# Kernel tuning notes

Hardware: AMD Instinct MI355X
Metric: run time of the kernel (lower is better)

The kernel has to match this reference:

```python
import jax, jax.numpy as jnp
import numpy as np

N_LAYERS = 2  # args.n_layers


def expmap0(u):
    """Hyperboloid (K=1/c, c=1) exponential map at the origin.
    u: [N, d] Euclidean tangent vector (spatial part; time coord is 0).
    Returns [N, d+1] point on the hyperboloid: (cosh||u||, sinh||u||*u/||u||).
    This matches Hyperboloid.expmap0(proj_tan0(cat([zeros, u], -1))) with c=1.
    """
    theta = jnp.sqrt(jnp.sum(u * u, axis=-1, keepdims=True))
    theta = jnp.maximum(theta, 1e-7)
    x0 = jnp.cosh(theta)
    xs = jnp.sinh(theta) * (u / theta)
    return jnp.concatenate([x0, xs], axis=-1)


def setup_inputs() -> dict:
    key = jax.random.key(0)
    k1, k2, k3, k4 = jax.random.split(key, 4)
    n_users, n_items, d, E = 100000, 150000, 64, 4000000
    N = n_users + n_items
    return {
        "user_emb": jax.random.normal(k1, (n_users, d), jnp.float32) * 0.1,
        "item_emb": jax.random.normal(k2, (n_items, d), jnp.float32) * 0.1,
        "h_list": jax.random.randint(k3, (E,), 0, N, dtype=jnp.int32),
        "t_list": jax.random.randint(k4, (E,), 0, N, dtype=jnp.int32),
    }


def reference(user_emb, item_emb, h_list, t_list):
    N = user_emb.shape[0] + item_emb.shape[0]
    dtype = user_emb.dtype

    # _cal_sparse_adj: symmetric normalization G = D^-1/2 A D^-1/2 in COO form
    deg = jax.ops.segment_sum(jnp.ones_like(h_list, dtype), h_list, num_segments=N)
    deg = jnp.maximum(deg, 1.0)
    g_values = jax.lax.rsqrt(deg[h_list] * deg[t_list])  # [E]

    # LightGCN-style propagation: x_{l+1} = G @ x_l, layer sum / mean
    x = jnp.concatenate([user_emb, item_emb], axis=0)  # [N, d]
    out = x
    for _ in range(N_LAYERS):
        msg = g_values[:, None] * x[t_list]              # [E, d] gather
        x = jax.ops.segment_sum(msg, h_list, num_segments=N)  # scatter-add SpMM
        out = out + x
    out = out / (N_LAYERS + 1)

    # Hyperbolic lift of the aggregated embeddings (zerou/zeroi + expmap0, c=1)
    h = expmap0(out)  # [N, d+1]

    return jnp.concatenate([out, h], axis=-1)  # [N, 2d+1]
```

## Files before the change

kernel.cpp:

```cpp
#include <hip/hip_runtime.h>

#define DIM 64
#define CHUNK 16384
#define BSHIFT 9
#define BSIZE (1 << BSHIFT)
#define MAXB 512
#define TBITS 21
#define TMASK ((1u << TBITS) - 1u)

__device__ __forceinline__ unsigned f2bf(float f) {
    unsigned u = __float_as_uint(f);
    return (u + 0x7FFFu + ((u >> 16) & 1u)) >> 16;
}
__device__ __forceinline__ float bflo(unsigned u) {
    return __uint_as_float(u << 16);
}
__device__ __forceinline__ float bfhi(unsigned u) {
    return __uint_as_float(u & 0xFFFF0000u);
}

__global__ void zero_u32(unsigned* __restrict__ p, int n) {
    int i = blockIdx.x * blockDim.x + threadIdx.x;
    int stride = gridDim.x * blockDim.x;
    for (; i < n; i += stride) p[i] = 0u;
}

__global__ void bucket_hist(const int* __restrict__ h, unsigned* __restrict__ bcount,
                            int E, int nb) {
    __shared__ unsigned s[MAXB];
    for (int i = threadIdx.x; i < nb; i += blockDim.x) s[i] = 0u;
    __syncthreads();
    int i = blockIdx.x * blockDim.x + threadIdx.x;
    int stride = gridDim.x * blockDim.x;
    for (; i < E; i += stride) atomicAdd(&s[((unsigned)h[i]) >> BSHIFT], 1u);
    __syncthreads();
    for (int i = threadIdx.x; i < nb; i += blockDim.x)
        if (s[i]) atomicAdd(&bcount[i], s[i]);
}

__global__ void bucket_scan(const unsigned* __restrict__ bcount,
                            unsigned* __restrict__ bbase, unsigned* __restrict__ bcur,
                            unsigned* __restrict__ row_ptr, int nb, int N, int E) {
    __shared__ unsigned s[MAXB];
    int tid = threadIdx.x;
    unsigned v = (tid < nb) ? bcount[tid] : 0u;
    s[tid] = v; __syncthreads();
    for (int off = 1; off < MAXB; off <<= 1) {
        unsigned t = (tid >= off) ? s[tid - off] : 0u;
        __syncthreads();
        s[tid] += t; __syncthreads();
    }
    if (tid < nb) {
        unsigned ex = s[tid] - v;
        bbase[tid] = ex;
        bcur[tid] = ex;
    }
    if (tid == 0) {
        bbase[nb] = (unsigned)E;
        row_ptr[N] = (unsigned)E;
    }
}

__global__ void partition_edges(const int* __restrict__ h, const int* __restrict__ t,
                                unsigned* __restrict__ bcur, unsigned* __restrict__ tmp,
                                int E, int nb) {
    __shared__ unsigned cnt[MAXB];
    int tid = threadIdx.x;
    long start = (long)blockIdx.x * CHUNK;
    long end = start + CHUNK; if (end > E) end = E;
    for (int i = tid; i < nb; i += blockDim.x) cnt[i] = 0u;
    __syncthreads();
    for (long i = start + tid; i < end; i += blockDim.x)
        atomicAdd(&cnt[((unsigned)h[i]) >> BSHIFT], 1u);
    __syncthreads();
    for (int i = tid; i < nb; i += blockDim.x) {
        unsigned c = cnt[i];
        cnt[i] = c ? atomicAdd(&bcur[i], c) : 0u;
    }
    __syncthreads();
    for (long i = start + tid; i < end; i += blockDim.x) {
        unsigned hn = (unsigned)h[i], tn = (unsigned)t[i];
        unsigned pos = atomicAdd(&cnt[hn >> BSHIFT], 1u);
        tmp[pos] = ((hn & (BSIZE - 1)) << TBITS) | tn;
    }
}

__global__ void build_csr_bucket(const unsigned* __restrict__ tmp,
                                 const unsigned* __restrict__ bbase,
                                 unsigned* __restrict__ row_ptr,
                                 float* __restrict__ rdeg,
                                 float* __restrict__ rsq,
                                 int* __restrict__ col,
                                 const float* __restrict__ ue,
                                 const float* __restrict__ ie,
                                 int n_users,
                                 unsigned short* __restrict__ x0s, int N) {
    __shared__ unsigned cnt[BSIZE];
    __shared__ unsigned cur[BSIZE];
    __shared__ unsigned ts[BSIZE];
    int b = blockIdx.x;
    int tid = threadIdx.x;
    unsigned e0 = bbase[b], e1 = bbase[b + 1];
    int nlo = b << BSHIFT;
    int nloc = N - nlo; if (nloc > BSIZE) nloc = BSIZE;
    cnt[tid] = 0u;
    __syncthreads();
    for (unsigned i = e0 + tid; i < e1; i += BSIZE)
        atomicAdd(&cnt[tmp[i] >> TBITS], 1u);
    __syncthreads();
    unsigned myc = cnt[tid];
    ts[tid] = myc; __syncthreads();
    for (int off = 1; off < BSIZE; off <<= 1) {
        unsigned t = (tid >= off) ? ts[tid - off] : 0u;
        __syncthreads();
        ts[tid] += t; __syncthreads();
    }
    unsigned off0 = ts[tid] - myc;
    if (tid < nloc) {
        float d = fmaxf((float)myc, 1.0f);
        cur[tid] = off0;
        row_ptr[nlo + tid] = e0 + off0;
        rdeg[nlo + tid] = rsqrtf(d);
        rsq[nlo + tid]  = sqrtf(d);
    }
    __syncthreads();
    for (unsigned i = e0 + tid; i < e1; i += BSIZE) {
        unsigned pk = tmp[i];
        unsigned pos = e0 + atomicAdd(&cur[pk >> TBITS], 1u);
        col[pos] = (int)(pk & TMASK);
    }
    long nu_elems = (long)n_users * DIM;
    int total = nloc * 16;
    for (int idx = tid; idx < total; idx += BSIZE) {
        int i = idx >> 4, j = idx & 15;
        long n = (long)(nlo + i);
        long elem = n * DIM + j * 4;
        const float* src = (elem < nu_elems) ? ue + elem : ie + (elem - nu_elems);
        float rd = rsqrtf(fmaxf((float)cnt[i], 1.0f));
        float4 v = *(const float4*)src;
        ushort4 o;
        o.x = (unsigned short)f2bf(rd * v.x); o.y = (unsigned short)f2bf(rd * v.y);
        o.z = (unsigned short)f2bf(rd * v.z); o.w = (unsigned short)f2bf(rd * v.w);
        *(ushort4*)(x0s + elem) = o;
    }
}

__global__ void spmm_pull_l1(const unsigned* __restrict__ rp,
                             const int* __restrict__ col,
                             const float* __restrict__ rdeg,
                             const uint4* __restrict__ x0s,
                             uint4* __restrict__ x1s, int N) {
    int node = blockIdx.x * (blockDim.x >> 3) + (threadIdx.x >> 3);
    int l = threadIdx.x & 7;
    if (node >= N) return;
    int e0 = (int)rp[node], e1 = (int)rp[node + 1];
    float a0 = 0.f, a1 = 0.f, a2 = 0.f, a3 = 0.f;
    float a4 = 0.f, a5 = 0.f, a6 = 0.f, a7 = 0.f;
    int e = e0;
    for (; e + 4 <= e1; e += 4) {
        int c0 = col[e], c1 = col[e + 1], c2 = col[e + 2], c3 = col[e + 3];
        uint4 u0 = x0s[((size_t)c0 << 3) + l];
        uint4 u1 = x0s[((size_t)c1 << 3) + l];
        uint4 u2 = x0s[((size_t)c2 << 3) + l];
        uint4 u3 = x0s[((size_t)c3 << 3) + l];
        a0 += bflo(u0.x) + bflo(u1.x) + bflo(u2.x) + bflo(u3.x);
        a1 += bfhi(u0.x) + bfhi(u1.x) + bfhi(u2.x) + bfhi(u3.x);
        a2 += bflo(u0.y) + bflo(u1.y) + bflo(u2.y) + bflo(u3.y);
        a3 += bfhi(u0.y) + bfhi(u1.y) + bfhi(u2.y) + bfhi(u3.y);
        a4 += bflo(u0.z) + bflo(u1.z) + bflo(u2.z) + bflo(u3.z);
        a5 += bfhi(u0.z) + bfhi(u1.z) + bfhi(u2.z) + bfhi(u3.z);
        a6 += bflo(u0.w) + bflo(u1.w) + bflo(u2.w) + bflo(u3.w);
        a7 += bfhi(u0.w) + bfhi(u1.w) + bfhi(u2.w) + bfhi(u3.w);
    }
    for (; e < e1; ++e) {
        int c = col[e];
        uint4 u = x0s[((size_t)c << 3) + l];
        a0 += bflo(u.x); a1 += bfhi(u.x);
        a2 += bflo(u.y); a3 += bfhi(u.y);
        a4 += bflo(u.z); a5 += bfhi(u.z);
        a6 += bflo(u.w); a7 += bfhi(u.w);
    }
    float rd = rdeg[node];
    float rd2 = rd * rd;
    uint4 o;
    o.x = (f2bf(rd2 * a1) << 16) | f2bf(rd2 * a0);
    o.y = (f2bf(rd2 * a3) << 16) | f2bf(rd2 * a2);
    o.z = (f2bf(rd2 * a5) << 16) | f2bf(rd2 * a4);
    o.w = (f2bf(rd2 * a7) << 16) | f2bf(rd2 * a6);
    x1s[((size_t)node << 3) + l] = o;
}

__global__ void spmm_l2_finalize(const unsigned* __restrict__ rp,
                                 const int* __restrict__ col,
                                 const float* __restrict__ rdeg,
                                 const float* __restrict__ rsq,
                                 const uint4* __restrict__ x0s,
                                 const uint4* __restrict__ x1s,
                                 float* __restrict__ out, int N) {
    int node = blockIdx.x * (blockDim.x >> 3) + (threadIdx.x >> 3);
    int l = threadIdx.x & 7;
    if (node >= N) return;
    int e0 = (int)rp[node], e1 = (int)rp[node + 1];
    float a0 = 0.f, a1 = 0.f, a2 = 0.f, a3 = 0.f;
    float a4 = 0.f, a5 = 0.f, a6 = 0.f, a7 = 0.f;
    int e = e0;
    for (; e + 4 <= e1; e += 4) {
        int c0 = col[e], c1 = col[e + 1], c2 = col[e + 2], c3 = col[e + 3];
        uint4 u0 = x1s[((size_t)c0 << 3) + l];
        uint4 u1 = x1s[((size_t)c1 << 3) + l];
        uint4 u2 = x1s[((size_t)c2 << 3) + l];
        uint4 u3 = x1s[((size_t)c3 << 3) + l];
        a0 += bflo(u0.x) + bflo(u1.x) + bflo(u2.x) + bflo(u3.x);
        a1 += bfhi(u0.x) + bfhi(u1.x) + bfhi(u2.x) + bfhi(u3.x);
        a2 += bflo(u0.y) + bflo(u1.y) + bflo(u2.y) + bflo(u3.y);
        a3 += bfhi(u0.y) + bfhi(u1.y) + bfhi(u2.y) + bfhi(u3.y);
        a4 += bflo(u0.z) + bflo(u1.z) + bflo(u2.z) + bflo(u3.z);
        a5 += bfhi(u0.z) + bfhi(u1.z) + bfhi(u2.z) + bfhi(u3.z);
        a6 += bflo(u0.w) + bflo(u1.w) + bflo(u2.w) + bflo(u3.w);
        a7 += bfhi(u0.w) + bfhi(u1.w) + bfhi(u2.w) + bfhi(u3.w);
    }
    for (; e < e1; ++e) {
        int c = col[e];
        uint4 u = x1s[((size_t)c << 3) + l];
        a0 += bflo(u.x); a1 += bfhi(u.x);
        a2 += bflo(u.y); a3 += bfhi(u.y);
        a4 += bflo(u.z); a5 += bfhi(u.z);
        a6 += bflo(u.w); a7 += bfhi(u.w);
    }
    float rd = rdeg[node];
    a0 *= rd; a1 *= rd; a2 *= rd; a3 *= rd;
    a4 *= rd; a5 *= rd; a6 *= rd; a7 *= rd;
    float rq = rsq[node];
    uint4 u0 = x0s[((size_t)node << 3) + l];
    uint4 u1 = x1s[((size_t)node << 3) + l];
    float v0 = (rq * (bflo(u0.x) + bflo(u1.x)) + a0) * (1.0f / 3.0f);
    float v1 = (rq * (bfhi(u0.x) + bfhi(u1.x)) + a1) * (1.0f / 3.0f);
    float v2 = (rq * (bflo(u0.y) + bflo(u1.y)) + a2) * (1.0f / 3.0f);
    float v3 = (rq * (bfhi(u0.y) + bfhi(u1.y)) + a3) * (1.0f / 3.0f);
    float v4 = (rq * (bflo(u0.z) + bflo(u1.z)) + a4) * (1.0f / 3.0f);
    float v5 = (rq * (bfhi(u0.z) + bfhi(u1.z)) + a5) * (1.0f / 3.0f);
    float v6 = (rq * (bflo(u0.w) + bflo(u1.w)) + a6) * (1.0f / 3.0f);
    float v7 = (rq * (bfhi(u0.w) + bfhi(u1.w)) + a7) * (1.0f / 3.0f);
    float ss = v0*v0 + v1*v1 + v2*v2 + v3*v3 + v4*v4 + v5*v5 + v6*v6 + v7*v7;
    ss += __shfl_xor(ss, 1);
    ss += __shfl_xor(ss, 2);
    ss += __shfl_xor(ss, 4);
    float theta = fmaxf(sqrtf(ss), 1e-7f);
    float ex  = __expf(theta);
    float exi = __builtin_amdgcn_rcpf(ex);
    float sh = 0.5f * (ex - exi);
    float ch = 0.5f * (ex + exi);
    float sc = sh * __builtin_amdgcn_rcpf(theta);
    float* o = out + (long)node * 129;
    *(float4*)(o + 8 * l)     = make_float4(v0, v1, v2, v3);
    *(float4*)(o + 8 * l + 4) = make_float4(v4, v5, v6, v7);
    if (l == 0) o[64] = ch;
    *(float4*)(o + 65 + 8 * l)     = make_float4(sc*v0, sc*v1, sc*v2, sc*v3);
    *(float4*)(o + 65 + 8 * l + 4) = make_float4(sc*v4, sc*v5, sc*v6, sc*v7);
}

extern "C" void kernel_launch(void* const* d_in, const int* in_sizes, int n_in,
                              void* d_out, int out_size, void* d_ws, size_t ws_size,
                              hipStream_t stream) {
    const float* ue = (const float*)d_in[0];
    const float* ie = (const float*)d_in[1];
    const int*   hl = (const int*)d_in[2];
    const int*   tl = (const int*)d_in[3];
    float* out = (float*)d_out;

    const int n_users = in_sizes[0] / DIM;
    const int n_items = in_sizes[1] / DIM;
    const int N = n_users + n_items;
    const int E = in_sizes[2];
    const int nb = (N + BSIZE - 1) >> BSHIFT;
    const long M = (long)N * DIM;

    auto align = [](size_t x) { return (x + 255) & ~(size_t)255; };
    char* p = (char*)d_ws;
    unsigned* row_ptr = (unsigned*)p;            p += align((size_t)(N + 1) * 4);
    float*    rdeg    = (float*)p;               p += align((size_t)N * 4);
    float*    rsq     = (float*)p;               p += align((size_t)N * 4);
    unsigned* bcount  = (unsigned*)p;            p += align((size_t)MAXB * 4);
    unsigned* bbase   = (unsigned*)p;            p += align((size_t)(MAXB + 1) * 4);
    unsigned* bcur    = (unsigned*)p;            p += align((size_t)MAXB * 4);
    int*      col     = (int*)p;                 p += align((size_t)E * 4);
    unsigned* tmp     = (unsigned*)p;            p += align((size_t)E * 4);
    unsigned short* x0sh = (unsigned short*)p;   p += align((size_t)M * 2);
    unsigned short* x1sh = (unsigned short*)p;
    const uint4* x0s = (const uint4*)x0sh;
    uint4* x1s = (uint4*)x1sh;

    zero_u32<<<1, 256, 0, stream>>>(bcount, MAXB);

    bucket_hist<<<512, 256, 0, stream>>>(hl, bcount, E, nb);

    bucket_scan<<<1, MAXB, 0, stream>>>(bcount, bbase, bcur, row_ptr, nb, N, E);

    {
        int blocks = (E + CHUNK - 1) / CHUNK;
        partition_edges<<<blocks, 256, 0, stream>>>(hl, tl, bcur, tmp, E, nb);
    }

    build_csr_bucket<<<nb, BSIZE, 0, stream>>>(tmp, bbase, row_ptr, rdeg, rsq, col,
                                               ue, ie, n_users, x0sh, N);

    {
        int nodes_per_block = 256 / 8;
        int blocks = (N + nodes_per_block - 1) / nodes_per_block;
        spmm_pull_l1<<<blocks, 256, 0, stream>>>(row_ptr, col, rdeg, x0s, x1s, N);
    }

    {
        int nodes_per_block = 256 / 8;
        int blocks = (N + nodes_per_block - 1) / nodes_per_block;
        spmm_l2_finalize<<<blocks, 256, 0, stream>>>(row_ptr, col, rdeg, rsq,
                                                     x0s, x1s, out, N);
    }
}
```

Baseline: 324.5 us.

## Fuse CSR build stages into one cooperative kernel with grid syncs

Replaces the zero, histogram, scan, partition and bucket-CSR kernels with a single cooperative kernel of nb blocks that uses grid.sync between phases. Each block computes its local bucket histogram once and keeps it in shared memory for the partition step, so the head array is no longer read twice for counting. This removes several kernel launches and gaps between them. In exchange it needs all blocks to be co-resident, adds grid-wide barrier costs, and ties the edge split to the bucket count.

New measurement: 527.4 us. +62.5%, slower.

```diff
diff --git a/kernel.cpp b/kernel.cpp
--- a/kernel.cpp
+++ b/kernel.cpp
@@ -1,7 +1,9 @@
 #include <hip/hip_runtime.h>
+#include <hip/hip_cooperative_groups.h>
+
+namespace cg = cooperative_groups;
 
 #define DIM 64
-#define CHUNK 16384
 #define BSHIFT 9
 #define BSIZE (1 << BSHIFT)
 #define MAXB 512
@@ -19,129 +21,116 @@
     return __uint_as_float(u & 0xFFFF0000u);
 }
 
-__global__ void zero_u32(unsigned* __restrict__ p, int n) {
-    int i = blockIdx.x * blockDim.x + threadIdx.x;
-    int stride = gridDim.x * blockDim.x;
-    for (; i < n; i += stride) p[i] = 0u;
-}
-
-__global__ void bucket_hist(const int* __restrict__ h, unsigned* __restrict__ bcount,
-                            int E, int nb) {
-    __shared__ unsigned s[MAXB];
-    for (int i = threadIdx.x; i < nb; i += blockDim.x) s[i] = 0u;
+__global__ void build_all(const int* __restrict__ h, const int* __restrict__ t,
+                          unsigned* __restrict__ bcount,
+                          unsigned* __restrict__ bbase, unsigned* __restrict__ bcur,
+                          unsigned* __restrict__ tmp,
+                          unsigned* __restrict__ row_ptr,
+                          float* __restrict__ rdeg, float* __restrict__ rsq,
+                          int* __restrict__ col,
+                          const float* __restrict__ ue, const float* __restrict__ ie,
+                          int n_users, unsigned short* __restrict__ x0s,
+                          int N, int E, int nb) {
+    cg::grid_group grid = cg::this_grid();
+    __shared__ unsigned sA[MAXB];
+    __shared__ unsigned sB[MAXB];
+    __shared__ unsigned sC[MAXB];
+    int bid = blockIdx.x;
+    int tid = threadIdx.x;
+
+    int per = (E + nb - 1) / nb;
+    long start = (long)bid * per;
+    long end = start + per; if (end > E) end = E;
+
+    if (bid == 0) bcount[tid] = 0u;
+    sA[tid] = 0u;
     __syncthreads();
-    int i = blockIdx.x * blockDim.x + threadIdx.x;
-    int stride = gridDim.x * blockDim.x;
-    for (; i < E; i += stride) atomicAdd(&s[((unsigned)h[i]) >> BSHIFT], 1u);
+    for (long i = start + tid; i < end; i += MAXB)
+        atomicAdd(&sA[((unsigned)h[i]) >> BSHIFT], 1u);
     __syncthreads();
-    for (int i = threadIdx.x; i < nb; i += blockDim.x)
-        if (s[i]) atomicAdd(&bcount[i], s[i]);
-}
-
-__global__ void bucket_scan(const unsigned* __restrict__ bcount,
-                            unsigned* __restrict__ bbase, unsigned* __restrict__ bcur,
-                            unsigned* __restrict__ row_ptr, int nb, int N, int E) {
-    __shared__ unsigned s[MAXB];
-    int tid = threadIdx.x;
-    unsigned v = (tid < nb) ? bcount[tid] : 0u;
-    s[tid] = v; __syncthreads();
-    for (int off = 1; off < MAXB; off <<= 1) {
-        unsigned t = (tid >= off) ? s[tid - off] : 0u;
-        __syncthreads();
-        s[tid] += t; __syncthreads();
-    }
-    if (tid < nb) {
-        unsigned ex = s[tid] - v;
-        bbase[tid] = ex;
-        bcur[tid] = ex;
-    }
-    if (tid == 0) {
-        bbase[nb] = (unsigned)E;
-        row_ptr[N] = (unsigned)E;
-    }
-}
-
-__global__ void partition_edges(const int* __restrict__ h, const int* __restrict__ t,
-                                unsigned* __restrict__ bcur, unsigned* __restrict__ tmp,
-                                int E, int nb) {
-    __shared__ unsigned cnt[MAXB];
-    int tid = threadIdx.x;
-    long start = (long)blockIdx.x * CHUNK;
-    long end = start + CHUNK; if (end > E) end = E;
-    for (int i = tid; i < nb; i += blockDim.x) cnt[i] = 0u;
-    __syncthreads();
-    for (long i = start + tid; i < end; i += blockDim.x)
-        atomicAdd(&cnt[((unsigned)h[i]) >> BSHIFT], 1u);
-    __syncthreads();
-    for (int i = tid; i < nb; i += blockDim.x) {
-        unsigned c = cnt[i];
-        cnt[i] = c ? atomicAdd(&bcur[i], c) : 0u;
-    }
-    __syncthreads();
-    for (long i = start + tid; i < end; i += blockDim.x) {
-        unsigned hn = (unsigned)h[i], tn = (unsigned)t[i];
-        unsigned pos = atomicAdd(&cnt[hn >> BSHIFT], 1u);
-        tmp[pos] = ((hn & (BSIZE - 1)) << TBITS) | tn;
-    }
-}
-
-__global__ void build_csr_bucket(const unsigned* __restrict__ tmp,
-                                 const unsigned* __restrict__ bbase,
-                                 unsigned* __restrict__ row_ptr,
-                                 float* __restrict__ rdeg,
-                                 float* __restrict__ rsq,
-                                 int* __restrict__ col,
-                                 const float* __restrict__ ue,
-                                 const float* __restrict__ ie,
-                                 int n_users,
-                                 unsigned short* __restrict__ x0s, int N) {
-    __shared__ unsigned cnt[BSIZE];
-    __shared__ unsigned cur[BSIZE];
-    __shared__ unsigned ts[BSIZE];
-    int b = blockIdx.x;
-    int tid = threadIdx.x;
-    unsigned e0 = bbase[b], e1 = bbase[b + 1];
-    int nlo = b << BSHIFT;
-    int nloc = N - nlo; if (nloc > BSIZE) nloc = BSIZE;
-    cnt[tid] = 0u;
-    __syncthreads();
-    for (unsigned i = e0 + tid; i < e1; i += BSIZE)
-        atomicAdd(&cnt[tmp[i] >> TBITS], 1u);
-    __syncthreads();
-    unsigned myc = cnt[tid];
-    ts[tid] = myc; __syncthreads();
-    for (int off = 1; off < BSIZE; off <<= 1) {
-        unsigned t = (tid >= off) ? ts[tid - off] : 0u;
-        __syncthreads();
-        ts[tid] += t; __syncthreads();
-    }
-    unsigned off0 = ts[tid] - myc;
-    if (tid < nloc) {
-        float d = fmaxf((float)myc, 1.0f);
-        cur[tid] = off0;
-        row_ptr[nlo + tid] = e0 + off0;
-        rdeg[nlo + tid] = rsqrtf(d);
-        rsq[nlo + tid]  = sqrtf(d);
-    }
-    __syncthreads();
-    for (unsigned i = e0 + tid; i < e1; i += BSIZE) {
-        unsigned pk = tmp[i];
-        unsigned pos = e0 + atomicAdd(&cur[pk >> TBITS], 1u);
-        col[pos] = (int)(pk & TMASK);
-    }
-    long nu_elems = (long)n_users * DIM;
-    int total = nloc * 16;
-    for (int idx = tid; idx < total; idx += BSIZE) {
-        int i = idx >> 4, j = idx & 15;
-        long n = (long)(nlo + i);
-        long elem = n * DIM + j * 4;
-        const float* src = (elem < nu_elems) ? ue + elem : ie + (elem - nu_elems);
-        float rd = rsqrtf(fmaxf((float)cnt[i], 1.0f));
-        float4 v = *(const float4*)src;
-        ushort4 o;
-        o.x = (unsigned short)f2bf(rd * v.x); o.y = (unsigned short)f2bf(rd * v.y);
-        o.z = (unsigned short)f2bf(rd * v.z); o.w = (unsigned short)f2bf(rd * v.w);
-        *(ushort4*)(x0s + elem) = o;
+    grid.sync();
+
+    if (sA[tid]) atomicAdd(&bcount[tid], sA[tid]);
+    grid.sync();
+
+    if (bid == 0) {
+        unsigned v = (tid < nb) ? bcount[tid] : 0u;
+        sC[tid] = v; __syncthreads();
+        for (int off = 1; off < MAXB; off <<= 1) {
+            unsigned tt = (tid >= off) ? sC[tid - off] : 0u;
+            __syncthreads();
+            sC[tid] += tt; __syncthreads();
+        }
+        if (tid < nb) {
+            unsigned ex = sC[tid] - v;
+            bbase[tid] = ex;
+            bcur[tid] = ex;
+        }
+        if (tid == 0) {
+            bbase[nb] = (unsigned)E;
+            row_ptr[N] = (unsigned)E;
+        }
+    }
+    grid.sync();
+
+    {
+        unsigned c = sA[tid];
+        unsigned base = c ? atomicAdd(&bcur[tid], c) : 0u;
+        __syncthreads();
+        sA[tid] = base;
+        __syncthreads();
+        for (long i = start + tid; i < end; i += MAXB) {
+            unsigned hn = (unsigned)h[i], tn = (unsigned)t[i];
+            unsigned pos = atomicAdd(&sA[hn >> BSHIFT], 1u);
+            tmp[pos] = ((hn & (BSIZE - 1)) << TBITS) | tn;
+        }
+    }
+    grid.sync();
+
+    {
+        unsigned e0 = bbase[bid], e1 = bbase[bid + 1];
+        int nlo = bid << BSHIFT;
+        int nloc = N - nlo; if (nloc > BSIZE) nloc = BSIZE;
+        sA[tid] = 0u;
+        __syncthreads();
+        for (unsigned i = e0 + tid; i < e1; i += BSIZE)
+            atomicAdd(&sA[tmp[i] >> TBITS], 1u);
+        __syncthreads();
+        unsigned myc = sA[tid];
+        sC[tid] = myc; __syncthreads();
+        for (int off = 1; off < BSIZE; off <<= 1) {
+            unsigned tt = (tid >= off) ? sC[tid - off] : 0u;
+            __syncthreads();
+            sC[tid] += tt; __syncthreads();
+        }
+        unsigned off0 = sC[tid] - myc;
+        if (tid < nloc) {
+            float d = fmaxf((float)myc, 1.0f);
+            sB[tid] = off0;
+            row_ptr[nlo + tid] = e0 + off0;
+            rdeg[nlo + tid] = rsqrtf(d);
+            rsq[nlo + tid]  = sqrtf(d);
+        }
+        __syncthreads();
+        for (unsigned i = e0 + tid; i < e1; i += BSIZE) {
+            unsigned pk = tmp[i];
+            unsigned pos = e0 + atomicAdd(&sB[pk >> TBITS], 1u);
+            col[pos] = (int)(pk & TMASK);
+        }
+        long nu_elems = (long)n_users * DIM;
+        int total = nloc * 16;
+        for (int idx = tid; idx < total; idx += BSIZE) {
+            int i = idx >> 4, j = idx & 15;
+            long n = (long)(nlo + i);
+            long elem = n * DIM + j * 4;
+            const float* src = (elem < nu_elems) ? ue + elem : ie + (elem - nu_elems);
+            float rd = rsqrtf(fmaxf((float)sA[i], 1.0f));
+            float4 v = *(const float4*)src;
+            ushort4 o;
+            o.x = (unsigned short)f2bf(rd * v.x); o.y = (unsigned short)f2bf(rd * v.y);
+            o.z = (unsigned short)f2bf(rd * v.z); o.w = (unsigned short)f2bf(rd * v.w);
+            *(ushort4*)(x0s + elem) = o;
+        }
     }
 }
 
@@ -268,11 +257,11 @@
     const int*   tl = (const int*)d_in[3];
     float* out = (float*)d_out;
 
-    const int n_users = in_sizes[0] / DIM;
+    int n_users = in_sizes[0] / DIM;
     const int n_items = in_sizes[1] / DIM;
-    const int N = n_users + n_items;
-    const int E = in_sizes[2];
-    const int nb = (N + BSIZE - 1) >> BSHIFT;
+    int N = n_users + n_items;
+    int E = in_sizes[2];
+    int nb = (N + BSIZE - 1) >> BSHIFT;
     const long M = (long)N * DIM;
 
     auto align = [](size_t x) { return (x + 255) & ~(size_t)255; };
@@ -290,19 +279,15 @@
     const uint4* x0s = (const uint4*)x0sh;
     uint4* x1s = (uint4*)x1sh;
 
-    zero_u32<<<1, 256, 0, stream>>>(bcount, MAXB);
-
-    bucket_hist<<<512, 256, 0, stream>>>(hl, bcount, E, nb);
-
-    bucket_scan<<<1, MAXB, 0, stream>>>(bcount, bbase, bcur, row_ptr, nb, N, E);
-
-    {
-        int blocks = (E + CHUNK - 1) / CHUNK;
-        partition_edges<<<blocks, 256, 0, stream>>>(hl, tl, bcur, tmp, E, nb);
-    }
-
-    build_csr_bucket<<<nb, BSIZE, 0, stream>>>(tmp, bbase, row_ptr, rdeg, rsq, col,
-                                               ue, ie, n_users, x0sh, N);
+    {
+        void* args[] = { (void*)&hl, (void*)&tl, (void*)&bcount, (void*)&bbase,
+                         (void*)&bcur, (void*)&tmp, (void*)&row_ptr, (void*)&rdeg,
+                         (void*)&rsq, (void*)&col, (void*)&ue, (void*)&ie,
+                         (void*)&n_users, (void*)&x0sh, (void*)&N, (void*)&E,
+                         (void*)&nb };
+        hipLaunchCooperativeKernel((const void*)build_all, dim3(nb), dim3(MAXB),
+                                   args, 0, stream);
+    }
 
     {
         int nodes_per_block = 256 / 8;
```
